# Optimization experiments

Measured on AMD Instinct MI355X. Metric: run time of the kernel, lower is better.

## Reference

```python
import jax, jax.numpy as jnp
import numpy as np

B, TE, TD, HE, HD = 8, 256, 128, 512, 512


def setup_inputs() -> dict:
    key = jax.random.key(0)
    k1, k2, k3, k4, k5 = jax.random.split(key, 5)
    # scale weights down (original uses 'uniform' init) to keep tanh unsaturated
    return {
        "encoder_out_seq": jax.random.normal(k1, (B, TE, HE), dtype=jnp.float32),
        "decoder_out_seq": jax.random.normal(k2, (B, TD, HD), dtype=jnp.float32),
        "W_a": jax.random.normal(k3, (HE, HE), dtype=jnp.float32) * 0.05,
        "U_a": jax.random.normal(k4, (HD, HE), dtype=jnp.float32) * 0.05,
        "V_a": jax.random.normal(k5, (HE, 1), dtype=jnp.float32) * 0.05,
    }


def reference(encoder_out_seq, decoder_out_seq, W_a, U_a, V_a):
    # Bahdanau additive attention, vectorized over all decoder timesteps
    # (the original loops over Td via K.rnn; steps are independent).
    Ws = jnp.einsum('bte,eh->bth', encoder_out_seq, W_a)   # [B, Te, He]
    Uh = jnp.einsum('bdk,kh->bdh', decoder_out_seq, U_a)   # [B, Td, He]
    # tanh(S.Wa + h.Ua): broadcast to [B, Td, Te, He], contract with V_a
    act = jnp.tanh(Ws[:, None, :, :] + Uh[:, :, None, :])  # [B, Td, Te, He]
    e = jnp.einsum('bdth,ho->bdt', act, V_a)                # [B, Td, Te]
    e = jax.nn.softmax(e, axis=-1)                          # attention weights
    c = jnp.einsum('bdt,bth->bdh', e, encoder_out_seq)      # [B, Td, He] contexts
    return (c, e)
```

## Files before the change

### kernel.cpp

```cpp
#include <hip/hip_runtime.h>

#define B_  8
#define TE_ 256
#define TD_ 128
#define HE_ 512

typedef __attribute__((ext_vector_type(8))) short short8v;
typedef __attribute__((ext_vector_type(4))) float f32x4;

#define C2 2.8853900817779268f

__device__ __forceinline__ float wave_red_add(float s) {
#define DPPADD(CTRL) \
  s += __int_as_float(__builtin_amdgcn_update_dpp(0, __float_as_int(s), CTRL, 0xf, 0xf, true))
  DPPADD(0x111);
  DPPADD(0x112);
  DPPADD(0x114);
  DPPADD(0x118);
  DPPADD(0x142);
  DPPADD(0x143);
#undef DPPADD
  return s;
}

__global__ __launch_bounds__(512) void gemm_fused(
    const float* __restrict__ enc, const float* __restrict__ dec,
    const float* __restrict__ Wa, const float* __restrict__ Ua,
    float* __restrict__ C) {
  __shared__ short BT[2][32][512];
  const int bid = blockIdx.x;
  const int mt = bid % 24, nt = bid / 24;
  const int m0 = mt * 128, n0 = nt * 32;
  const bool isenc = (mt < 16);
  const float* Bsrc = isenc ? Wa : Ua;
  const float* Asrc = isenc ? enc + (size_t)m0 * 512
                            : dec + (size_t)(m0 - 2048) * 512;
  const int tid = threadIdx.x;
  {
    const int kp = tid >> 3;
    const int c4 = (tid & 7) * 4;
    for (int p = 0; p < 4; ++p) {
      const int k = 2 * kp + p * 128;
      float4 v0 = *(const float4*)(Bsrc + (size_t)k * 512 + n0 + c4);
      float4 v1 = *(const float4*)(Bsrc + (size_t)(k + 1) * 512 + n0 + c4);
      const float a0[4] = {v0.x, v0.y, v0.z, v0.w};
      const float a1[4] = {v1.x, v1.y, v1.z, v1.w};
      const int kc = k >> 3, klo = k & 7;
#pragma unroll
      for (int q = 0; q < 4; ++q) {
        const int n = c4 + q;
        unsigned u0 = __float_as_uint(a0[q]);
        unsigned u1 = __float_as_uint(a1[q]);
        unsigned hi32 = __builtin_amdgcn_perm(u1, u0, 0x07060302);
        float l0 = a0[q] - __uint_as_float(u0 & 0xffff0000u);
        float l1 = a1[q] - __uint_as_float(u1 & 0xffff0000u);
        unsigned lo32 = __builtin_amdgcn_perm(__float_as_uint(l1), __float_as_uint(l0), 0x07060302);
        const int slot = (kc & ~7) | ((kc ^ n) & 7);
        *(unsigned*)&BT[0][n][slot * 8 + klo] = hi32;
        *(unsigned*)&BT[1][n][slot * 8 + klo] = lo32;
      }
    }
  }
  __syncthreads();
  const int w = tid >> 6, lane = tid & 63;
  const int fm = lane & 15, fc = lane >> 4;
  const float* Ap = Asrc + (size_t)(w * 16 + fm) * 512 + fc * 8;
  f32x4 acc0 = {}, acc1 = {};
  float4 pfa[2], pfb[2];
  pfa[0] = *(const float4*)(Ap);
  pfb[0] = *(const float4*)(Ap + 4);
  pfa[1] = *(const float4*)(Ap + 32);
  pfb[1] = *(const float4*)(Ap + 36);
  for (int it = 0; it < 16; ++it) {
    const float4 fa = pfa[it & 1];
    const float4 fb = pfb[it & 1];
    if (it < 14) {
      pfa[it & 1] = *(const float4*)(Ap + (it + 2) * 32);
      pfb[it & 1] = *(const float4*)(Ap + (it + 2) * 32 + 4);
    }
    const float af[8] = {fa.x, fa.y, fa.z, fa.w, fb.x, fb.y, fb.z, fb.w};
    union { unsigned u[4]; short8v s; } ahu, alu;
#pragma unroll
    for (int e = 0; e < 4; ++e) {
      unsigned u0 = __float_as_uint(af[2 * e]);
      unsigned u1 = __float_as_uint(af[2 * e + 1]);
      ahu.u[e] = __builtin_amdgcn_perm(u1, u0, 0x07060302);
      float l0 = af[2 * e]     - __uint_as_float(u0 & 0xffff0000u);
      float l1 = af[2 * e + 1] - __uint_as_float(u1 & 0xffff0000u);
      alu.u[e] = __builtin_amdgcn_perm(__float_as_uint(l1), __float_as_uint(l0), 0x07060302);
    }
    const short8v ah = ahu.s, al = alu.s;
    const int kc = it * 4 + fc;
    const int base = kc & ~7;
    const int s0 = (base | ((kc ^ fm) & 7)) * 8;
    const int s1 = (base | ((kc ^ (16 + fm)) & 7)) * 8;
    short8v bh0 = *(const short8v*)&BT[0][fm][s0];
    short8v bl0 = *(const short8v*)&BT[1][fm][s0];
    short8v bh1 = *(const short8v*)&BT[0][16 + fm][s1];
    short8v bl1 = *(const short8v*)&BT[1][16 + fm][s1];
    acc0 = __builtin_amdgcn_mfma_f32_16x16x32_bf16(ah, bh0, acc0, 0, 0, 0);
    acc1 = __builtin_amdgcn_mfma_f32_16x16x32_bf16(ah, bh1, acc1, 0, 0, 0);
    acc0 = __builtin_amdgcn_mfma_f32_16x16x32_bf16(ah, bl0, acc0, 0, 0, 0);
    acc1 = __builtin_amdgcn_mfma_f32_16x16x32_bf16(ah, bl1, acc1, 0, 0, 0);
    acc0 = __builtin_amdgcn_mfma_f32_16x16x32_bf16(al, bh0, acc0, 0, 0, 0);
    acc1 = __builtin_amdgcn_mfma_f32_16x16x32_bf16(al, bh1, acc1, 0, 0, 0);
  }
  const int row = m0 + w * 16 + fc * 4;
  float* Cp = C + (size_t)row * 512 + n0 + fm;
  if (isenc) {
#pragma unroll
    for (int r = 0; r < 4; ++r)
      Cp[(size_t)r * 512] = __builtin_amdgcn_exp2f(C2 * acc0[r]);
#pragma unroll
    for (int r = 0; r < 4; ++r)
      Cp[(size_t)r * 512 + 16] = __builtin_amdgcn_exp2f(C2 * acc1[r]);
  } else {
#pragma unroll
    for (int r = 0; r < 4; ++r) Cp[(size_t)r * 512] = acc0[r];
#pragma unroll
    for (int r = 0; r < 4; ++r) Cp[(size_t)r * 512 + 16] = acc1[r];
  }
}

__global__ __launch_bounds__(1024) void attn_fused(
    const float* __restrict__ EWs, const float* __restrict__ Uh,
    const float* __restrict__ Va, const float* __restrict__ enc,
    float* __restrict__ c_out, float* __restrict__ e_out) {
  __shared__ float sUh[2][HE_];
  __shared__ float sV[HE_];
  __shared__ float sE[2][TE_];
  __shared__ float sRed[8];
  __shared__ float sNorm[2];
  const int tid = threadIdx.x;
  const int b  = blockIdx.x & 7;
  const int d0 = (blockIdx.x >> 3) * 2;
  if (tid < 256)
    ((float4*)sUh)[tid] = ((const float4*)(Uh + (size_t)(b * TD_ + d0) * HE_))[tid];
  else if (tid < 384)
    ((float4*)sV)[tid - 256] = ((const float4*)Va)[tid - 256];
  __syncthreads();
  const int lane = tid & 63, w = tid >> 6;
  const int tb = w * 16;
  const int h0 = lane * 8;
  float eU[2][8], vv2[8], sumv = 0.f;
#pragma unroll
  for (int j = 0; j < 8; ++j) {
    const float vj = sV[h0 + j];
    sumv += vj;
    vv2[j] = 2.0f * vj;
    eU[0][j] = __builtin_amdgcn_exp2f(C2 * sUh[0][h0 + j]);
    eU[1][j] = __builtin_amdgcn_exp2f(C2 * sUh[1][h0 + j]);
  }
  const float* pw = EWs + ((size_t)b * TE_ + tb) * HE_ + h0;
  float4 a0 = *(const float4*)(pw);
  float4 a1 = *(const float4*)(pw + 4);
  float s0, s1;
#define TELT2(X, J) { \
    float E0 = (X) * eU[0][J]; \
    float E1 = (X) * eU[1][J]; \
    float r0 = __builtin_amdgcn_rcpf(E0 + 1.0f); \
    float r1 = __builtin_amdgcn_rcpf(E1 + 1.0f); \
    s0 = fmaf(-vv2[J], r0, s0); s1 = fmaf(-vv2[J], r1, s1); }
  for (int ti = 0; ti < 16; ++ti) {
    const float* pn = pw + HE_;
    float4 n0 = *(const float4*)(pn);
    float4 n1 = *(const float4*)(pn + 4);
    s0 = s1 = sumv;
    TELT2(a0.x, 0) TELT2(a0.y, 1) TELT2(a0.z, 2) TELT2(a0.w, 3)
    TELT2(a1.x, 4) TELT2(a1.y, 5) TELT2(a1.z, 6) TELT2(a1.w, 7)
    s0 = wave_red_add(s0);
    s1 = wave_red_add(s1);
    if (lane == 63) {
      sE[0][tb + ti] = s0;
      sE[1][tb + ti] = s1;
    }
    a0 = n0; a1 = n1;
    pw = pn;
  }
  __syncthreads();
  if (tid < 512) {
    const int dA = tid >> 8, t = tid & 255;
    const float ex = __expf(sE[dA][t]);
    float sum = wave_red_add(ex);
    if (lane == 63) sRed[w] = sum;
    __syncthreads();
    if (tid < 2)
      sNorm[tid] = 1.0f / (sRed[tid * 4] + sRed[tid * 4 + 1] + sRed[tid * 4 + 2] + sRed[tid * 4 + 3]);
    __syncthreads();
    const float wgt = ex * sNorm[dA];
    sE[dA][t] = wgt;
    e_out[(size_t)(b * TD_ + d0 + dA) * TE_ + t] = wgt;
  } else {
    __syncthreads();
    __syncthreads();
  }
  __syncthreads();
  const int h = tid & 511;
  const int dd = tid >> 9;
  float acc = 0.f;
  const float* ep = enc + (size_t)b * TE_ * HE_ + h;
  const float* ew = sE[dd];
#pragma unroll 8
  for (int tt = 0; tt < TE_; ++tt)
    acc = fmaf(ew[tt], ep[(size_t)tt * HE_], acc);
  c_out[(size_t)(b * TD_ + d0 + dd) * HE_ + h] = acc;
}

extern "C" void kernel_launch(void* const* d_in, const int* in_sizes, int n_in,
                              void* d_out, int out_size, void* d_ws, size_t ws_size,
                              hipStream_t stream) {
  const float* enc = (const float*)d_in[0];
  const float* dec = (const float*)d_in[1];
  const float* Wa  = (const float*)d_in[2];
  const float* Ua  = (const float*)d_in[3];
  const float* Va  = (const float*)d_in[4];
  float* c_out = (float*)d_out;
  float* e_out = c_out + (size_t)B_ * TD_ * HE_;
  float* Cws = (float*)d_ws;
  const float* EWs = Cws;
  const float* Uh  = Cws + (size_t)2048 * 512;
  gemm_fused<<<384, 512, 0, stream>>>(enc, dec, Wa, Ua, Cws);
  attn_fused<<<512, 1024, 0, stream>>>(EWs, Uh, Va, enc, c_out, e_out);
}
```

Measured before the change: 117.3 us.

## Move context GEMM to a separate MFMA kernel and precompute exp of Uh

```diff
diff --git a/kernel.cpp b/kernel.cpp
--- a/kernel.cpp
+++ b/kernel.cpp
@@ -107,26 +107,18 @@
   }
   const int row = m0 + w * 16 + fc * 4;
   float* Cp = C + (size_t)row * 512 + n0 + fm;
-  if (isenc) {
-#pragma unroll
-    for (int r = 0; r < 4; ++r)
-      Cp[(size_t)r * 512] = __builtin_amdgcn_exp2f(C2 * acc0[r]);
-#pragma unroll
-    for (int r = 0; r < 4; ++r)
-      Cp[(size_t)r * 512 + 16] = __builtin_amdgcn_exp2f(C2 * acc1[r]);
-  } else {
-#pragma unroll
-    for (int r = 0; r < 4; ++r) Cp[(size_t)r * 512] = acc0[r];
-#pragma unroll
-    for (int r = 0; r < 4; ++r) Cp[(size_t)r * 512 + 16] = acc1[r];
-  }
+#pragma unroll
+  for (int r = 0; r < 4; ++r)
+    Cp[(size_t)r * 512] = __builtin_amdgcn_exp2f(C2 * acc0[r]);
+#pragma unroll
+  for (int r = 0; r < 4; ++r)
+    Cp[(size_t)r * 512 + 16] = __builtin_amdgcn_exp2f(C2 * acc1[r]);
 }
 
 __global__ __launch_bounds__(1024) void attn_fused(
-    const float* __restrict__ EWs, const float* __restrict__ Uh,
-    const float* __restrict__ Va, const float* __restrict__ enc,
-    float* __restrict__ c_out, float* __restrict__ e_out) {
-  __shared__ float sUh[2][HE_];
+    const float* __restrict__ EWs, const float* __restrict__ EU,
+    const float* __restrict__ Va, float* __restrict__ e_out) {
+  __shared__ float sEU[2][HE_];
   __shared__ float sV[HE_];
   __shared__ float sE[2][TE_];
   __shared__ float sRed[8];
@@ -135,7 +127,7 @@
   const int b  = blockIdx.x & 7;
   const int d0 = (blockIdx.x >> 3) * 2;
   if (tid < 256)
-    ((float4*)sUh)[tid] = ((const float4*)(Uh + (size_t)(b * TD_ + d0) * HE_))[tid];
+    ((float4*)sEU)[tid] = ((const float4*)(EU + (size_t)(b * TD_ + d0) * HE_))[tid];
   else if (tid < 384)
     ((float4*)sV)[tid - 256] = ((const float4*)Va)[tid - 256];
   __syncthreads();
@@ -148,8 +140,8 @@
     const float vj = sV[h0 + j];
     sumv += vj;
     vv2[j] = 2.0f * vj;
-    eU[0][j] = __builtin_amdgcn_exp2f(C2 * sUh[0][h0 + j]);
-    eU[1][j] = __builtin_amdgcn_exp2f(C2 * sUh[1][h0 + j]);
+    eU[0][j] = sEU[0][h0 + j];
+    eU[1][j] = sEU[1][h0 + j];
   }
   const float* pw = EWs + ((size_t)b * TE_ + tb) * HE_ + h0;
   float4 a0 = *(const float4*)(pw);
@@ -187,23 +179,89 @@
     if (tid < 2)
       sNorm[tid] = 1.0f / (sRed[tid * 4] + sRed[tid * 4 + 1] + sRed[tid * 4 + 2] + sRed[tid * 4 + 3]);
     __syncthreads();
-    const float wgt = ex * sNorm[dA];
-    sE[dA][t] = wgt;
-    e_out[(size_t)(b * TD_ + d0 + dA) * TE_ + t] = wgt;
+    e_out[(size_t)(b * TD_ + d0 + dA) * TE_ + t] = ex * sNorm[dA];
   } else {
     __syncthreads();
     __syncthreads();
   }
-  __syncthreads();
-  const int h = tid & 511;
-  const int dd = tid >> 9;
-  float acc = 0.f;
-  const float* ep = enc + (size_t)b * TE_ * HE_ + h;
-  const float* ew = sE[dd];
-#pragma unroll 8
-  for (int tt = 0; tt < TE_; ++tt)
-    acc = fmaf(ew[tt], ep[(size_t)tt * HE_], acc);
-  c_out[(size_t)(b * TD_ + d0 + dd) * HE_ + h] = acc;
+}
+
+__global__ __launch_bounds__(512) void ctx_gemm(
+    const float* __restrict__ e, const float* __restrict__ enc,
+    float* __restrict__ c_out) {
+  __shared__ short BT[2][32][256];
+  const int bid = blockIdx.x;
+  const int b = bid & 7, nt = bid >> 3;
+  const int n0 = nt * 32;
+  const float* A    = e   + (size_t)b * TD_ * TE_;
+  const float* Bsrc = enc + (size_t)b * TE_ * HE_;
+  const int tid = threadIdx.x;
+  {
+    const int kp = tid >> 3;
+    const int c4 = (tid & 7) * 4;
+    for (int p = 0; p < 2; ++p) {
+      const int k = 2 * kp + p * 128;
+      float4 v0 = *(const float4*)(Bsrc + (size_t)k * HE_ + n0 + c4);
+      float4 v1 = *(const float4*)(Bsrc + (size_t)(k + 1) * HE_ + n0 + c4);
+      const float a0[4] = {v0.x, v0.y, v0.z, v0.w};
+      const float a1[4] = {v1.x, v1.y, v1.z, v1.w};
+      const int kc = k >> 3, klo = k & 7;
+#pragma unroll
+      for (int q = 0; q < 4; ++q) {
+        const int n = c4 + q;
+        unsigned u0 = __float_as_uint(a0[q]);
+        unsigned u1 = __float_as_uint(a1[q]);
+        unsigned hi32 = __builtin_amdgcn_perm(u1, u0, 0x07060302);
+        float l0 = a0[q] - __uint_as_float(u0 & 0xffff0000u);
+        float l1 = a1[q] - __uint_as_float(u1 & 0xffff0000u);
+        unsigned lo32 = __builtin_amdgcn_perm(__float_as_uint(l1), __float_as_uint(l0), 0x07060302);
+        const int slot = (kc & ~7) | ((kc ^ n) & 7);
+        *(unsigned*)&BT[0][n][slot * 8 + klo] = hi32;
+        *(unsigned*)&BT[1][n][slot * 8 + klo] = lo32;
+      }
+    }
+  }
+  __syncthreads();
+  const int w = tid >> 6, lane = tid & 63;
+  const int fm = lane & 15, fc = lane >> 4;
+  const float* Ap = A + (size_t)(w * 16 + fm) * TE_ + fc * 8;
+  f32x4 acc0 = {}, acc1 = {};
+  for (int it = 0; it < 8; ++it) {
+    const float4 fa = *(const float4*)(Ap + it * 32);
+    const float4 fb = *(const float4*)(Ap + it * 32 + 4);
+    const float af[8] = {fa.x, fa.y, fa.z, fa.w, fb.x, fb.y, fb.z, fb.w};
+    union { unsigned u[4]; short8v s; } ahu, alu;
+#pragma unroll
+    for (int q = 0; q < 4; ++q) {
+      unsigned u0 = __float_as_uint(af[2 * q]);
+      unsigned u1 = __float_as_uint(af[2 * q + 1]);
+      ahu.u[q] = __builtin_amdgcn_perm(u1, u0, 0x07060302);
+      float l0 = af[2 * q]     - __uint_as_float(u0 & 0xffff0000u);
+      float l1 = af[2 * q + 1] - __uint_as_float(u1 & 0xffff0000u);
+      alu.u[q] = __builtin_amdgcn_perm(__float_as_uint(l1), __float_as_uint(l0), 0x07060302);
+    }
+    const short8v ah = ahu.s, al = alu.s;
+    const int kc = it * 4 + fc;
+    const int base = kc & ~7;
+    const int s0 = (base | ((kc ^ fm) & 7)) * 8;
+    const int s1 = (base | ((kc ^ (16 + fm)) & 7)) * 8;
+    short8v bh0 = *(const short8v*)&BT[0][fm][s0];
+    short8v bl0 = *(const short8v*)&BT[1][fm][s0];
+    short8v bh1 = *(const short8v*)&BT[0][16 + fm][s1];
+    short8v bl1 = *(const short8v*)&BT[1][16 + fm][s1];
+    acc0 = __builtin_amdgcn_mfma_f32_16x16x32_bf16(ah, bh0, acc0, 0, 0, 0);
+    acc1 = __builtin_amdgcn_mfma_f32_16x16x32_bf16(ah, bh1, acc1, 0, 0, 0);
+    acc0 = __builtin_amdgcn_mfma_f32_16x16x32_bf16(ah, bl0, acc0, 0, 0, 0);
+    acc1 = __builtin_amdgcn_mfma_f32_16x16x32_bf16(ah, bl1, acc1, 0, 0, 0);
+    acc0 = __builtin_amdgcn_mfma_f32_16x16x32_bf16(al, bh0, acc0, 0, 0, 0);
+    acc1 = __builtin_amdgcn_mfma_f32_16x16x32_bf16(al, bh1, acc1, 0, 0, 0);
+  }
+  const int row = w * 16 + fc * 4;
+  float* Cp = c_out + (size_t)(b * TD_ + row) * HE_ + n0 + fm;
+#pragma unroll
+  for (int r = 0; r < 4; ++r) Cp[(size_t)r * HE_] = acc0[r];
+#pragma unroll
+  for (int r = 0; r < 4; ++r) Cp[(size_t)r * HE_ + 16] = acc1[r];
 }
 
 extern "C" void kernel_launch(void* const* d_in, const int* in_sizes, int n_in,
@@ -218,7 +276,8 @@
   float* e_out = c_out + (size_t)B_ * TD_ * HE_;
   float* Cws = (float*)d_ws;
   const float* EWs = Cws;
-  const float* Uh  = Cws + (size_t)2048 * 512;
+  const float* EU  = Cws + (size_t)2048 * 512;
   gemm_fused<<<384, 512, 0, stream>>>(enc, dec, Wa, Ua, Cws);
-  attn_fused<<<512, 1024, 0, stream>>>(EWs, Uh, Va, enc, c_out, e_out);
-}
+  attn_fused<<<512, 1024, 0, stream>>>(EWs, EU, Va, e_out);
+  ctx_gemm<<<128, 512, 0, stream>>>(e_out, enc, c_out);
+}
```

Result: faster. 110.0 us (-6.2%).
